# Performance work log

Measured on AMD Instinct MI355X. Metric: run time of the kernel, lower is better.

The kernel has to match this reference:

```python
import jax, jax.numpy as jnp
import numpy as np

D_MODEL, H, D_K, D_V = 512, 8, 64, 64
S_Q, S_KV = 2048, 2048


def setup_inputs() -> dict:
    key = jax.random.key(0)
    ks = jax.random.split(key, 11)
    sc = 0.02
    return {
        "embeddings": jax.random.normal(ks[0], (S_Q, D_MODEL), jnp.float32),
        "K": jax.random.normal(ks[1], (S_KV, D_MODEL), jnp.float32),
        "V": jax.random.normal(ks[2], (S_KV, D_MODEL), jnp.float32),
        # per-head projection weights (stacked over heads) + biases
        "Wq": jax.random.normal(ks[3], (H, D_MODEL, D_K), jnp.float32) * sc,
        "bq": jax.random.normal(ks[4], (H, D_K), jnp.float32) * sc,
        "Wk": jax.random.normal(ks[5], (H, D_MODEL, D_K), jnp.float32) * sc,
        "bk": jax.random.normal(ks[6], (H, D_K), jnp.float32) * sc,
        "Wv": jax.random.normal(ks[7], (H, D_MODEL, D_V), jnp.float32) * sc,
        "bv": jax.random.normal(ks[8], (H, D_V), jnp.float32) * sc,
        # final linear: [h*d_v -> d_model]
        "Wo": jax.random.normal(ks[9], (H * D_V, D_MODEL), jnp.float32) * sc,
        "bo": jax.random.normal(ks[10], (D_MODEL,), jnp.float32) * sc,
    }


def reference(embeddings, K, V, Wq, bq, Wk, bk, Wv, bv, Wo, bo):
    # Batched per-head projections (the original loops over h heads; math identical)
    q = jnp.einsum("sd,hdk->hsk", embeddings, Wq) + bq[:, None, :]  # [h, Sq, d_k]
    k = jnp.einsum("td,hdk->htk", K, Wk) + bk[:, None, :]           # [h, Skv, d_k]
    v = jnp.einsum("td,hdv->htv", V, Wv) + bv[:, None, :]           # [h, Skv, d_v]
    scores = jnp.einsum("hsk,htk->hst", q, k) / jnp.sqrt(jnp.asarray(D_K, q.dtype))
    attn = jax.nn.softmax(scores, axis=-1)                           # [h, Sq, Skv]
    out = jnp.einsum("hst,htv->hsv", attn, v)                        # [h, Sq, d_v]
    # torch.cat(results, dim=1): head 0's d_v columns first -> [Sq, h*d_v]
    concat = jnp.transpose(out, (1, 0, 2)).reshape(S_Q, H * D_V)
    return concat @ Wo + bo                                          # [Sq, d_model]
```

## Files before the change

### kernel.cpp

```cpp
#include <hip/hip_runtime.h>

#define SQ 2048
#define DM 512
#define NH 8
#define NSPLIT 4

typedef __bf16 bf16x8 __attribute__((ext_vector_type(8)));
typedef float f32x4 __attribute__((ext_vector_type(4)));
typedef unsigned short us8 __attribute__((ext_vector_type(8)));
typedef unsigned short us4 __attribute__((ext_vector_type(4)));

__device__ __forceinline__ unsigned short f2bf(float f) {
    unsigned u = __builtin_bit_cast(unsigned, f);
    u += 0x7fffu + ((u >> 16) & 1u);
    return (unsigned short)(u >> 16);
}
__device__ __forceinline__ float bf2f(unsigned short u) {
    return __builtin_bit_cast(float, (unsigned)u << 16);
}

__global__ __launch_bounds__(256) void convert_w(
    const float* __restrict__ Wq,  const float* __restrict__ Wk,  const float* __restrict__ Wv,
    const float* __restrict__ Wo,
    unsigned short* __restrict__ Wt,
    unsigned short* __restrict__ Woth, unsigned short* __restrict__ Wotl)
{
    const int b = blockIdx.x, tid = threadIdx.x;
    __shared__ float ld[64 * 68];
    float4* ld4 = reinterpret_cast<float4*>(ld);

    if (b < 192) {
        const int wi = b;
        const int idx = wi >> 3;
        const int kt = wi & 7;
        const int p = idx >> 3, h = idx & 7;
        const float* src = ((p == 0) ? Wq : (p == 1) ? Wk : Wv)
                         + (size_t)h * 512 * 64 + (size_t)kt * 64 * 64;
        unsigned short* dst = Wt + (size_t)idx * 64 * 512 + kt * 64;
        const int rr = tid >> 4, c4 = tid & 15;
        #pragma unroll
        for (int it = 0; it < 4; it++) {
            int r = rr + 16 * it;
            ld4[r * 17 + c4] = reinterpret_cast<const float4*>(src + (size_t)r * 64)[c4];
        }
        __syncthreads();
        #pragma unroll
        for (int it = 0; it < 2; it++) {
            int slot = tid + it * 256;
            int n = slot >> 3, g = slot & 7;
            us8 o;
            #pragma unroll
            for (int i = 0; i < 8; i++)
                o[i] = f2bf(ld[(g * 8 + i) * 68 + n]);
            *reinterpret_cast<us8*>(dst + (size_t)n * 512 + g * 8) = o;
        }
    } else {
        const int ti = b - 192;
        const int kt = ti >> 3, nt = ti & 7;
        const float* src = Wo + (size_t)kt * 64 * 512 + nt * 64;
        const int rr = tid >> 4, c4 = tid & 15;
        #pragma unroll
        for (int it = 0; it < 4; it++) {
            int r = rr + 16 * it;
            ld4[r * 17 + c4] = reinterpret_cast<const float4*>(src + (size_t)r * 512)[c4];
        }
        __syncthreads();
        #pragma unroll
        for (int it = 0; it < 2; it++) {
            int slot = tid + it * 256;
            int n = slot >> 3, g = slot & 7;
            us8 oh, ol;
            #pragma unroll
            for (int i = 0; i < 8; i++) {
                float v = ld[(g * 8 + i) * 68 + n];
                unsigned short hi = f2bf(v);
                oh[i] = hi;
                ol[i] = f2bf(v - bf2f(hi));
            }
            size_t doff = (size_t)(nt * 64 + n) * 512 + kt * 64 + g * 8;
            *reinterpret_cast<us8*>(Woth + doff) = oh;
            *reinterpret_cast<us8*>(Wotl + doff) = ol;
        }
    }
}

__global__ __launch_bounds__(256) void qkv_mfma(
    const float* __restrict__ emb, const float* __restrict__ Kin,
    const float* __restrict__ Vin, const unsigned short* __restrict__ Wt,
    const float* __restrict__ bq, const float* __restrict__ bk, const float* __restrict__ bv,
    unsigned short* __restrict__ qo, unsigned short* __restrict__ ko, unsigned short* __restrict__ vo)
{
    const int p = blockIdx.z, h = blockIdx.y, s0 = blockIdx.x * 64;
    const float* X = (p == 0) ? emb : (p == 1) ? Kin : Vin;
    const unsigned short* W = Wt + (size_t)(p * 8 + h) * 64 * 512;
    const float* B = ((p == 0) ? bq : (p == 1) ? bk : bv) + h * 64;

    const int tid = threadIdx.x;
    const int w = tid >> 6, lane = tid & 63, cl = lane & 15, q4 = lane >> 4;
    const int sr = tid >> 3, sg = tid & 7;

    __shared__ unsigned short As[2][64 * 72];
    __shared__ unsigned short Bs[2][64 * 72];

    #pragma unroll
    for (int it = 0; it < 2; it++) {
        int r = sr + 32 * it;
        const float4* xs = reinterpret_cast<const float4*>(&X[(size_t)(s0 + r) * 512 + sg * 8]);
        float4 f0 = xs[0], f1 = xs[1];
        us8 o;
        o[0] = f2bf(f0.x); o[1] = f2bf(f0.y); o[2] = f2bf(f0.z); o[3] = f2bf(f0.w);
        o[4] = f2bf(f1.x); o[5] = f2bf(f1.y); o[6] = f2bf(f1.z); o[7] = f2bf(f1.w);
        *reinterpret_cast<us8*>(&As[0][r * 72 + sg * 8]) = o;
        *reinterpret_cast<float4*>(&Bs[0][r * 72 + sg * 8]) =
            *reinterpret_cast<const float4*>(&W[(size_t)r * 512 + sg * 8]);
    }

    f32x4 acc[4] = {};

    for (int c = 0; c < 8; c++) {
        __syncthreads();
        const int buf = c & 1;
        const bool more = (c + 1 < 8);
        float4 ar[2][2], br[2];
        if (more) {
            #pragma unroll
            for (int it = 0; it < 2; it++) {
                int r = sr + 32 * it;
                const float4* xs = reinterpret_cast<const float4*>(
                    &X[(size_t)(s0 + r) * 512 + (c + 1) * 64 + sg * 8]);
                ar[it][0] = xs[0];
                ar[it][1] = xs[1];
                br[it] = *reinterpret_cast<const float4*>(
                    &W[(size_t)r * 512 + (c + 1) * 64 + sg * 8]);
            }
        }

        bf16x8 a0 = *reinterpret_cast<const bf16x8*>(&As[buf][(16 * w + cl) * 72 + q4 * 8]);
        bf16x8 a1 = *reinterpret_cast<const bf16x8*>(&As[buf][(16 * w + cl) * 72 + 32 + q4 * 8]);
        #pragma unroll
        for (int nn = 0; nn < 4; nn++) {
            bf16x8 b0 = *reinterpret_cast<const bf16x8*>(&Bs[buf][(16 * nn + cl) * 72 + q4 * 8]);
            bf16x8 b1 = *reinterpret_cast<const bf16x8*>(&Bs[buf][(16 * nn + cl) * 72 + 32 + q4 * 8]);
            acc[nn] = __builtin_amdgcn_mfma_f32_16x16x32_bf16(a0, b0, acc[nn], 0, 0, 0);
            acc[nn] = __builtin_amdgcn_mfma_f32_16x16x32_bf16(a1, b1, acc[nn], 0, 0, 0);
        }

        if (more) {
            const int nbuf = buf ^ 1;
            #pragma unroll
            for (int it = 0; it < 2; it++) {
                int r = sr + 32 * it;
                us8 o;
                o[0] = f2bf(ar[it][0].x); o[1] = f2bf(ar[it][0].y);
                o[2] = f2bf(ar[it][0].z); o[3] = f2bf(ar[it][0].w);
                o[4] = f2bf(ar[it][1].x); o[5] = f2bf(ar[it][1].y);
                o[6] = f2bf(ar[it][1].z); o[7] = f2bf(ar[it][1].w);
                *reinterpret_cast<us8*>(&As[nbuf][r * 72 + sg * 8]) = o;
                *reinterpret_cast<float4*>(&Bs[nbuf][r * 72 + sg * 8]) = br[it];
            }
        }
    }

    if (p == 0) {
        const float QSCALE = 0.125f * 1.4426950408889634f;
        #pragma unroll
        for (int nn = 0; nn < 4; nn++) {
            int col = 16 * nn + cl;
            float bb = B[col];
            #pragma unroll
            for (int r = 0; r < 4; r++)
                qo[((size_t)h * SQ + s0 + 16 * w + q4 * 4 + r) * 64 + col] =
                    f2bf((acc[nn][r] + bb) * QSCALE);
        }
    } else if (p == 1) {
        #pragma unroll
        for (int nn = 0; nn < 4; nn++) {
            int col = 16 * nn + cl;
            float bb = B[col];
            #pragma unroll
            for (int r = 0; r < 4; r++)
                ko[((size_t)h * SQ + s0 + 16 * w + q4 * 4 + r) * 64 + col] =
                    f2bf(acc[nn][r] + bb);
        }
    } else {
        #pragma unroll
        for (int nn = 0; nn < 4; nn++) {
            int col = 16 * nn + cl;
            float bb = B[col];
            ushort4 o;
            o.x = f2bf(acc[nn][0] + bb);
            o.y = f2bf(acc[nn][1] + bb);
            o.z = f2bf(acc[nn][2] + bb);
            o.w = f2bf(acc[nn][3] + bb);
            *reinterpret_cast<ushort4*>(
                vo + ((size_t)h * 64 + col) * SQ + s0 + 16 * w + q4 * 4) = o;
        }
    }
}

#define PW 72

__global__ __launch_bounds__(256, 4) void attn_fwd(
    const unsigned short* __restrict__ qbf,
    const unsigned short* __restrict__ kbf,
    const unsigned short* __restrict__ vbf,
    float* __restrict__ Opart,
    float* __restrict__ lpart)
{
    const int h = blockIdx.y, s0 = blockIdx.x * 64, z = blockIdx.z;
    const int tid = threadIdx.x;
    const int w = tid >> 6, lane = tid & 63, cl = lane & 15, q4 = lane >> 4;
    const int NT = SQ / 64 / NSPLIT;
    const int t0 = z * NT;

    __shared__ unsigned short Ks[2][64 * PW];
    __shared__ unsigned short Vs[2][64 * PW];

    bf16x8 aq0 = *reinterpret_cast<const bf16x8*>(
        &qbf[((size_t)h * SQ + s0 + 16 * w + cl) * 64 + q4 * 8]);
    bf16x8 aq1 = *reinterpret_cast<const bf16x8*>(
        &qbf[((size_t)h * SQ + s0 + 16 * w + cl) * 64 + 32 + q4 * 8]);

    const int sr = tid >> 3, sg = tid & 7;
    const int kapA = 32 * (sg >> 2) + 16 * (sg & 1) + 4 * ((sg >> 1) & 1);

    #pragma unroll
    for (int it = 0; it < 2; it++) {
        int r = sr + 32 * it;
        *reinterpret_cast<float4*>(&Ks[0][r * PW + sg * 8]) =
            *reinterpret_cast<const float4*>(&kbf[((size_t)h * SQ + t0 * 64 + r) * 64 + sg * 8]);
        us8 vv = *reinterpret_cast<const us8*>(&vbf[((size_t)h * 64 + r) * SQ + t0 * 64 + sg * 8]);
        *reinterpret_cast<us4*>(&Vs[0][r * PW + kapA]) =
            __builtin_shufflevector(vv, vv, 0, 1, 2, 3);
        *reinterpret_cast<us4*>(&Vs[0][r * PW + kapA + 8]) =
            __builtin_shufflevector(vv, vv, 4, 5, 6, 7);
    }

    f32x4 o_acc[4] = {};
    float lsum = 0.f;

    for (int tl = 0; tl < NT; tl++) {
        __syncthreads();
        const int buf = tl & 1;
        const bool more = (tl + 1 < NT);
        float4 kr[2];
        us8 vr[2];
        if (more) {
            #pragma unroll
            for (int it = 0; it < 2; it++) {
                int r = sr + 32 * it;
                kr[it] = *reinterpret_cast<const float4*>(
                    &kbf[((size_t)h * SQ + (t0 + tl + 1) * 64 + r) * 64 + sg * 8]);
                vr[it] = *reinterpret_cast<const us8*>(
                    &vbf[((size_t)h * 64 + r) * SQ + (t0 + tl + 1) * 64 + sg * 8]);
            }
        }

        f32x4 s_acc[4] = {};
        #pragma unroll
        for (int nn = 0; nn < 4; nn++) {
            bf16x8 k0 = *reinterpret_cast<const bf16x8*>(&Ks[buf][(16 * nn + cl) * PW + q4 * 8]);
            bf16x8 k1 = *reinterpret_cast<const bf16x8*>(&Ks[buf][(16 * nn + cl) * PW + 32 + q4 * 8]);
            s_acc[nn] = __builtin_amdgcn_mfma_f32_16x16x32_bf16(k0, aq0, s_acc[nn], 0, 0, 0);
            s_acc[nn] = __builtin_amdgcn_mfma_f32_16x16x32_bf16(k1, aq1, s_acc[nn], 0, 0, 0);
        }

        bf16x8 ap0, ap1;
        #pragma unroll
        for (int nn = 0; nn < 4; nn++) {
            #pragma unroll
            for (int r = 0; r < 4; r++) {
                float pv = __builtin_amdgcn_exp2f(s_acc[nn][r]);
                lsum += pv;
                if (nn < 2) ap0[nn * 4 + r] = (__bf16)pv;
                else        ap1[(nn - 2) * 4 + r] = (__bf16)pv;
            }
        }

        #pragma unroll
        for (int nn = 0; nn < 4; nn++) {
            bf16x8 b0 = *reinterpret_cast<const bf16x8*>(&Vs[buf][(16 * nn + cl) * PW + q4 * 8]);
            bf16x8 b1 = *reinterpret_cast<const bf16x8*>(&Vs[buf][(16 * nn + cl) * PW + 32 + q4 * 8]);
            o_acc[nn] = __builtin_amdgcn_mfma_f32_16x16x32_bf16(ap0, b0, o_acc[nn], 0, 0, 0);
            o_acc[nn] = __builtin_amdgcn_mfma_f32_16x16x32_bf16(ap1, b1, o_acc[nn], 0, 0, 0);
        }

        if (more) {
            const int nbuf = buf ^ 1;
            #pragma unroll
            for (int it = 0; it < 2; it++) {
                int r = sr + 32 * it;
                *reinterpret_cast<float4*>(&Ks[nbuf][r * PW + sg * 8]) = kr[it];
                *reinterpret_cast<us4*>(&Vs[nbuf][r * PW + kapA]) =
                    __builtin_shufflevector(vr[it], vr[it], 0, 1, 2, 3);
                *reinterpret_cast<us4*>(&Vs[nbuf][r * PW + kapA + 8]) =
                    __builtin_shufflevector(vr[it], vr[it], 4, 5, 6, 7);
            }
        }
    }

    lsum += __shfl_xor(lsum, 16);
    lsum += __shfl_xor(lsum, 32);

    const size_t zb = (size_t)(z * NH + h);
    if (q4 == 0)
        lpart[zb * SQ + s0 + 16 * w + cl] = lsum;

    #pragma unroll
    for (int nn = 0; nn < 4; nn++)
        #pragma unroll
        for (int r = 0; r < 4; r++)
            Opart[(zb * SQ + s0 + 16 * w + q4 * 4 + r) * 64 + 16 * nn + cl] = o_acc[nn][r];
}

__global__ __launch_bounds__(256) void attn_combine(
    const float* __restrict__ Opart, const float* __restrict__ lpart,
    unsigned short* __restrict__ athi, unsigned short* __restrict__ atlo)
{
    const int gid = blockIdx.x * 256 + threadIdx.x;
    const int s = gid >> 6, oct = gid & 63;
    const int col0 = oct * 8, h = col0 >> 6, dv0 = col0 & 63;

    float l = 0.f;
    #pragma unroll
    for (int z = 0; z < NSPLIT; z++)
        l += lpart[(size_t)(z * NH + h) * SQ + s];
    const float inv = 1.0f / l;

    float o[8] = {};
    #pragma unroll
    for (int z = 0; z < NSPLIT; z++) {
        const float4* base = reinterpret_cast<const float4*>(
            Opart + ((size_t)(z * NH + h) * SQ + s) * 64 + dv0);
        float4 a = base[0], bq = base[1];
        o[0] += a.x; o[1] += a.y; o[2] += a.z; o[3] += a.w;
        o[4] += bq.x; o[5] += bq.y; o[6] += bq.z; o[7] += bq.w;
    }
    us8 hi, lo;
    #pragma unroll
    for (int i = 0; i < 8; i++) {
        float v = o[i] * inv;
        unsigned short hb = f2bf(v);
        hi[i] = hb;
        lo[i] = f2bf(v - bf2f(hb));
    }
    *reinterpret_cast<us8*>(athi + (size_t)s * DM + col0) = hi;
    *reinterpret_cast<us8*>(atlo + (size_t)s * DM + col0) = lo;
}

__global__ __launch_bounds__(256) void out_proj(
    const unsigned short* __restrict__ ah, const unsigned short* __restrict__ al,
    const unsigned short* __restrict__ Wh, const unsigned short* __restrict__ Wl,
    const float* __restrict__ bo, float* __restrict__ out)
{
    const int s0 = blockIdx.x * 64, n0 = blockIdx.y * 64;
    const int tid = threadIdx.x;
    const int w = tid >> 6, lane = tid & 63, cl = lane & 15, q4 = lane >> 4;
    const int sr = tid >> 3, sg = tid & 7;

    __shared__ unsigned short Ah[2][64 * 72], Al[2][64 * 72];
    __shared__ unsigned short Bh[2][64 * 72], Bl[2][64 * 72];

    #pragma unroll
    for (int it = 0; it < 2; it++) {
        int r = sr + 32 * it;
        *reinterpret_cast<float4*>(&Ah[0][r * 72 + sg * 8]) =
            *reinterpret_cast<const float4*>(&ah[(size_t)(s0 + r) * 512 + sg * 8]);
        *reinterpret_cast<float4*>(&Al[0][r * 72 + sg * 8]) =
            *reinterpret_cast<const float4*>(&al[(size_t)(s0 + r) * 512 + sg * 8]);
        *reinterpret_cast<float4*>(&Bh[0][r * 72 + sg * 8]) =
            *reinterpret_cast<const float4*>(&Wh[(size_t)(n0 + r) * 512 + sg * 8]);
        *reinterpret_cast<float4*>(&Bl[0][r * 72 + sg * 8]) =
            *reinterpret_cast<const float4*>(&Wl[(size_t)(n0 + r) * 512 + sg * 8]);
    }

    f32x4 acc[4] = {};

    for (int c = 0; c < 8; c++) {
        __syncthreads();
        const int buf = c & 1;
        const bool more = (c + 1 < 8);
        float4 ahr[2], alr[2], bhr[2], blr[2];
        if (more) {
            #pragma unroll
            for (int it = 0; it < 2; it++) {
                int r = sr + 32 * it;
                int off = (c + 1) * 64 + sg * 8;
                ahr[it] = *reinterpret_cast<const float4*>(&ah[(size_t)(s0 + r) * 512 + off]);
                alr[it] = *reinterpret_cast<const float4*>(&al[(size_t)(s0 + r) * 512 + off]);
                bhr[it] = *reinterpret_cast<const float4*>(&Wh[(size_t)(n0 + r) * 512 + off]);
                blr[it] = *reinterpret_cast<const float4*>(&Wl[(size_t)(n0 + r) * 512 + off]);
            }
        }

        bf16x8 ah0 = *reinterpret_cast<const bf16x8*>(&Ah[buf][(16 * w + cl) * 72 + q4 * 8]);
        bf16x8 ah1 = *reinterpret_cast<const bf16x8*>(&Ah[buf][(16 * w + cl) * 72 + 32 + q4 * 8]);
        bf16x8 al0 = *reinterpret_cast<const bf16x8*>(&Al[buf][(16 * w + cl) * 72 + q4 * 8]);
        bf16x8 al1 = *reinterpret_cast<const bf16x8*>(&Al[buf][(16 * w + cl) * 72 + 32 + q4 * 8]);
        #pragma unroll
        for (int nn = 0; nn < 4; nn++) {
            bf16x8 bh0 = *reinterpret_cast<const bf16x8*>(&Bh[buf][(16 * nn + cl) * 72 + q4 * 8]);
            bf16x8 bh1 = *reinterpret_cast<const bf16x8*>(&Bh[buf][(16 * nn + cl) * 72 + 32 + q4 * 8]);
            bf16x8 bl0 = *reinterpret_cast<const bf16x8*>(&Bl[buf][(16 * nn + cl) * 72 + q4 * 8]);
            bf16x8 bl1 = *reinterpret_cast<const bf16x8*>(&Bl[buf][(16 * nn + cl) * 72 + 32 + q4 * 8]);
            acc[nn] = __builtin_amdgcn_mfma_f32_16x16x32_bf16(ah0, bh0, acc[nn], 0, 0, 0);
            acc[nn] = __builtin_amdgcn_mfma_f32_16x16x32_bf16(ah1, bh1, acc[nn], 0, 0, 0);
            acc[nn] = __builtin_amdgcn_mfma_f32_16x16x32_bf16(ah0, bl0, acc[nn], 0, 0, 0);
            acc[nn] = __builtin_amdgcn_mfma_f32_16x16x32_bf16(ah1, bl1, acc[nn], 0, 0, 0);
            acc[nn] = __builtin_amdgcn_mfma_f32_16x16x32_bf16(al0, bh0, acc[nn], 0, 0, 0);
            acc[nn] = __builtin_amdgcn_mfma_f32_16x16x32_bf16(al1, bh1, acc[nn], 0, 0, 0);
        }

        if (more) {
            const int nbuf = buf ^ 1;
            #pragma unroll
            for (int it = 0; it < 2; it++) {
                int r = sr + 32 * it;
                *reinterpret_cast<float4*>(&Ah[nbuf][r * 72 + sg * 8]) = ahr[it];
                *reinterpret_cast<float4*>(&Al[nbuf][r * 72 + sg * 8]) = alr[it];
                *reinterpret_cast<float4*>(&Bh[nbuf][r * 72 + sg * 8]) = bhr[it];
                *reinterpret_cast<float4*>(&Bl[nbuf][r * 72 + sg * 8]) = blr[it];
            }
        }
    }

    #pragma unroll
    for (int nn = 0; nn < 4; nn++) {
        int col = n0 + 16 * nn + cl;
        float bb = bo[col];
        #pragma unroll
        for (int r = 0; r < 4; r++)
            out[(size_t)(s0 + 16 * w + q4 * 4 + r) * DM + col] = acc[nn][r] + bb;
    }
}

extern "C" void kernel_launch(void* const* d_in, const int* in_sizes, int n_in,
                              void* d_out, int out_size, void* d_ws, size_t ws_size,
                              hipStream_t stream) {
    const float* emb = (const float*)d_in[0];
    const float* Kin = (const float*)d_in[1];
    const float* Vin = (const float*)d_in[2];
    const float* Wq  = (const float*)d_in[3];
    const float* bq  = (const float*)d_in[4];
    const float* Wk  = (const float*)d_in[5];
    const float* bk  = (const float*)d_in[6];
    const float* Wv  = (const float*)d_in[7];
    const float* bv  = (const float*)d_in[8];
    const float* Wo  = (const float*)d_in[9];
    const float* bo  = (const float*)d_in[10];
    float* out = (float*)d_out;

    unsigned short* p = (unsigned short*)d_ws;
    unsigned short* Wt   = p; p += (size_t)24 * 64 * 512;
    unsigned short* Woth = p; p += (size_t)512 * 512;
    unsigned short* Wotl = p; p += (size_t)512 * 512;
    unsigned short* qbf  = p; p += (size_t)NH * SQ * 64;
    unsigned short* kbf  = p; p += (size_t)NH * SQ * 64;
    unsigned short* vbf  = p; p += (size_t)NH * SQ * 64;
    unsigned short* athi = p; p += (size_t)SQ * DM;
    unsigned short* atlo = p; p += (size_t)SQ * DM;
    float* Opart = (float*)p;
    float* lpart = Opart + (size_t)NSPLIT * NH * SQ * 64;

    convert_w<<<256, 256, 0, stream>>>(Wq, Wk, Wv, Wo, Wt, Woth, Wotl);
    qkv_mfma<<<dim3(32, 8, 3), 256, 0, stream>>>(emb, Kin, Vin, Wt, bq, bk, bv,
                                                 qbf, kbf, vbf);
    attn_fwd<<<dim3(32, 8, NSPLIT), 256, 0, stream>>>(qbf, kbf, vbf, Opart, lpart);
    attn_combine<<<512, 256, 0, stream>>>(Opart, lpart, athi, atlo);
    out_proj<<<dim3(32, 8), 256, 0, stream>>>(athi, atlo, Woth, Wotl, bo, out);
}
```

Baseline: 120.5 us.

## Split attention KV tiles across wave pairs with two query subtiles per wave

Each wave now processes 32 query rows (two 16-row subtiles) against one of two KV tiles staged together, so each K/V fragment read from LDS feeds two MFMAs instead of one. The two wave pairs reduce their partial O and row sums through shared memory at the end. The register-prefetch double buffer is dropped in favour of synchronous staging of two tiles per iteration, which exposes global load latency and doubles accumulator register use.

```diff
diff --git a/kernel.cpp b/kernel.cpp
--- a/kernel.cpp
+++ b/kernel.cpp
@@ -210,107 +210,128 @@
     const int h = blockIdx.y, s0 = blockIdx.x * 64, z = blockIdx.z;
     const int tid = threadIdx.x;
     const int w = tid >> 6, lane = tid & 63, cl = lane & 15, q4 = lane >> 4;
+    const int qh = w >> 1, tp = w & 1;
     const int NT = SQ / 64 / NSPLIT;
     const int t0 = z * NT;
 
-    __shared__ unsigned short Ks[2][64 * PW];
-    __shared__ unsigned short Vs[2][64 * PW];
-
-    bf16x8 aq0 = *reinterpret_cast<const bf16x8*>(
-        &qbf[((size_t)h * SQ + s0 + 16 * w + cl) * 64 + q4 * 8]);
-    bf16x8 aq1 = *reinterpret_cast<const bf16x8*>(
-        &qbf[((size_t)h * SQ + s0 + 16 * w + cl) * 64 + 32 + q4 * 8]);
+    __shared__ unsigned short SH[4 * 64 * PW];
+
+    bf16x8 aq[2][2];
+    #pragma unroll
+    for (int qs = 0; qs < 2; qs++) {
+        const unsigned short* qb =
+            &qbf[((size_t)h * SQ + s0 + 32 * qh + 16 * qs + cl) * 64 + q4 * 8];
+        aq[qs][0] = *reinterpret_cast<const bf16x8*>(qb);
+        aq[qs][1] = *reinterpret_cast<const bf16x8*>(qb + 32);
+    }
 
     const int sr = tid >> 3, sg = tid & 7;
     const int kapA = 32 * (sg >> 2) + 16 * (sg & 1) + 4 * ((sg >> 1) & 1);
 
-    #pragma unroll
-    for (int it = 0; it < 2; it++) {
-        int r = sr + 32 * it;
-        *reinterpret_cast<float4*>(&Ks[0][r * PW + sg * 8]) =
-            *reinterpret_cast<const float4*>(&kbf[((size_t)h * SQ + t0 * 64 + r) * 64 + sg * 8]);
-        us8 vv = *reinterpret_cast<const us8*>(&vbf[((size_t)h * 64 + r) * SQ + t0 * 64 + sg * 8]);
-        *reinterpret_cast<us4*>(&Vs[0][r * PW + kapA]) =
-            __builtin_shufflevector(vv, vv, 0, 1, 2, 3);
-        *reinterpret_cast<us4*>(&Vs[0][r * PW + kapA + 8]) =
-            __builtin_shufflevector(vv, vv, 4, 5, 6, 7);
-    }
-
-    f32x4 o_acc[4] = {};
-    float lsum = 0.f;
-
-    for (int tl = 0; tl < NT; tl++) {
+    auto stage = [&](int par, int t) {
+        unsigned short* Kd = &SH[par * 64 * PW];
+        unsigned short* Vd = &SH[(2 + par) * 64 * PW];
+        #pragma unroll
+        for (int it = 0; it < 2; it++) {
+            int r = sr + 32 * it;
+            *reinterpret_cast<float4*>(&Kd[r * PW + sg * 8]) =
+                *reinterpret_cast<const float4*>(&kbf[((size_t)h * SQ + t * 64 + r) * 64 + sg * 8]);
+            us8 vv = *reinterpret_cast<const us8*>(&vbf[((size_t)h * 64 + r) * SQ + t * 64 + sg * 8]);
+            *reinterpret_cast<us4*>(&Vd[r * PW + kapA]) =
+                __builtin_shufflevector(vv, vv, 0, 1, 2, 3);
+            *reinterpret_cast<us4*>(&Vd[r * PW + kapA + 8]) =
+                __builtin_shufflevector(vv, vv, 4, 5, 6, 7);
+        }
+    };
+
+    stage(0, t0);
+    stage(1, t0 + 1);
+    __syncthreads();
+
+    f32x4 o_acc[2][4] = {};
+    float lsum[2] = {};
+    const unsigned short* Kb = &SH[tp * 64 * PW];
+    const unsigned short* Vb = &SH[(2 + tp) * 64 * PW];
+
+    for (int pr = 0; pr < NT / 2; pr++) {
+        f32x4 s_acc[2][4] = {};
+        #pragma unroll
+        for (int nn = 0; nn < 4; nn++) {
+            bf16x8 k0 = *reinterpret_cast<const bf16x8*>(&Kb[(16 * nn + cl) * PW + q4 * 8]);
+            bf16x8 k1 = *reinterpret_cast<const bf16x8*>(&Kb[(16 * nn + cl) * PW + 32 + q4 * 8]);
+            #pragma unroll
+            for (int qs = 0; qs < 2; qs++) {
+                s_acc[qs][nn] = __builtin_amdgcn_mfma_f32_16x16x32_bf16(k0, aq[qs][0], s_acc[qs][nn], 0, 0, 0);
+                s_acc[qs][nn] = __builtin_amdgcn_mfma_f32_16x16x32_bf16(k1, aq[qs][1], s_acc[qs][nn], 0, 0, 0);
+            }
+        }
+
+        bf16x8 ap[2][2];
+        #pragma unroll
+        for (int qs = 0; qs < 2; qs++)
+            #pragma unroll
+            for (int nn = 0; nn < 4; nn++)
+                #pragma unroll
+                for (int r = 0; r < 4; r++) {
+                    float pv = __builtin_amdgcn_exp2f(s_acc[qs][nn][r]);
+                    lsum[qs] += pv;
+                    ap[qs][nn >> 1][(nn & 1) * 4 + r] = (__bf16)pv;
+                }
+
+        #pragma unroll
+        for (int nn = 0; nn < 4; nn++) {
+            bf16x8 b0 = *reinterpret_cast<const bf16x8*>(&Vb[(16 * nn + cl) * PW + q4 * 8]);
+            bf16x8 b1 = *reinterpret_cast<const bf16x8*>(&Vb[(16 * nn + cl) * PW + 32 + q4 * 8]);
+            #pragma unroll
+            for (int qs = 0; qs < 2; qs++) {
+                o_acc[qs][nn] = __builtin_amdgcn_mfma_f32_16x16x32_bf16(ap[qs][0], b0, o_acc[qs][nn], 0, 0, 0);
+                o_acc[qs][nn] = __builtin_amdgcn_mfma_f32_16x16x32_bf16(ap[qs][1], b1, o_acc[qs][nn], 0, 0, 0);
+            }
+        }
+
         __syncthreads();
-        const int buf = tl & 1;
-        const bool more = (tl + 1 < NT);
-        float4 kr[2];
-        us8 vr[2];
-        if (more) {
-            #pragma unroll
-            for (int it = 0; it < 2; it++) {
-                int r = sr + 32 * it;
-                kr[it] = *reinterpret_cast<const float4*>(
-                    &kbf[((size_t)h * SQ + (t0 + tl + 1) * 64 + r) * 64 + sg * 8]);
-                vr[it] = *reinterpret_cast<const us8*>(
-                    &vbf[((size_t)h * 64 + r) * SQ + (t0 + tl + 1) * 64 + sg * 8]);
-            }
-        }
-
-        f32x4 s_acc[4] = {};
-        #pragma unroll
-        for (int nn = 0; nn < 4; nn++) {
-            bf16x8 k0 = *reinterpret_cast<const bf16x8*>(&Ks[buf][(16 * nn + cl) * PW + q4 * 8]);
-            bf16x8 k1 = *reinterpret_cast<const bf16x8*>(&Ks[buf][(16 * nn + cl) * PW + 32 + q4 * 8]);
-            s_acc[nn] = __builtin_amdgcn_mfma_f32_16x16x32_bf16(k0, aq0, s_acc[nn], 0, 0, 0);
-            s_acc[nn] = __builtin_amdgcn_mfma_f32_16x16x32_bf16(k1, aq1, s_acc[nn], 0, 0, 0);
-        }
-
-        bf16x8 ap0, ap1;
-        #pragma unroll
-        for (int nn = 0; nn < 4; nn++) {
-            #pragma unroll
-            for (int r = 0; r < 4; r++) {
-                float pv = __builtin_amdgcn_exp2f(s_acc[nn][r]);
-                lsum += pv;
-                if (nn < 2) ap0[nn * 4 + r] = (__bf16)pv;
-                else        ap1[(nn - 2) * 4 + r] = (__bf16)pv;
-            }
-        }
-
-        #pragma unroll
-        for (int nn = 0; nn < 4; nn++) {
-            bf16x8 b0 = *reinterpret_cast<const bf16x8*>(&Vs[buf][(16 * nn + cl) * PW + q4 * 8]);
-            bf16x8 b1 = *reinterpret_cast<const bf16x8*>(&Vs[buf][(16 * nn + cl) * PW + 32 + q4 * 8]);
-            o_acc[nn] = __builtin_amdgcn_mfma_f32_16x16x32_bf16(ap0, b0, o_acc[nn], 0, 0, 0);
-            o_acc[nn] = __builtin_amdgcn_mfma_f32_16x16x32_bf16(ap1, b1, o_acc[nn], 0, 0, 0);
-        }
-
-        if (more) {
-            const int nbuf = buf ^ 1;
-            #pragma unroll
-            for (int it = 0; it < 2; it++) {
-                int r = sr + 32 * it;
-                *reinterpret_cast<float4*>(&Ks[nbuf][r * PW + sg * 8]) = kr[it];
-                *reinterpret_cast<us4*>(&Vs[nbuf][r * PW + kapA]) =
-                    __builtin_shufflevector(vr[it], vr[it], 0, 1, 2, 3);
-                *reinterpret_cast<us4*>(&Vs[nbuf][r * PW + kapA + 8]) =
-                    __builtin_shufflevector(vr[it], vr[it], 4, 5, 6, 7);
-            }
-        }
-    }
-
-    lsum += __shfl_xor(lsum, 16);
-    lsum += __shfl_xor(lsum, 32);
-
-    const size_t zb = (size_t)(z * NH + h);
-    if (q4 == 0)
-        lpart[zb * SQ + s0 + 16 * w + cl] = lsum;
-
-    #pragma unroll
-    for (int nn = 0; nn < 4; nn++)
-        #pragma unroll
-        for (int r = 0; r < 4; r++)
-            Opart[(zb * SQ + s0 + 16 * w + q4 * 4 + r) * 64 + 16 * nn + cl] = o_acc[nn][r];
+        if (pr + 1 < NT / 2) {
+            stage(0, t0 + 2 * pr + 2);
+            stage(1, t0 + 2 * pr + 3);
+            __syncthreads();
+        }
+    }
+
+    __syncthreads();
+    float* Ox = reinterpret_cast<float*>(SH);
+    float* Lx = Ox + 4096;
+    if (tp == 1) {
+        #pragma unroll
+        for (int qs = 0; qs < 2; qs++) {
+            #pragma unroll
+            for (int nn = 0; nn < 4; nn++)
+                *reinterpret_cast<f32x4*>(&Ox[(((qh * 2 + qs) * 4 + nn) * 256) + lane * 4]) =
+                    o_acc[qs][nn];
+            Lx[(qh * 2 + qs) * 64 + lane] = lsum[qs];
+        }
+    }
+    __syncthreads();
+    if (tp == 0) {
+        const size_t zb = (size_t)(z * NH + h);
+        #pragma unroll
+        for (int qs = 0; qs < 2; qs++) {
+            #pragma unroll
+            for (int nn = 0; nn < 4; nn++)
+                o_acc[qs][nn] += *reinterpret_cast<const f32x4*>(
+                    &Ox[(((qh * 2 + qs) * 4 + nn) * 256) + lane * 4]);
+            float v = lsum[qs] + Lx[(qh * 2 + qs) * 64 + lane];
+            v += __shfl_xor(v, 16);
+            v += __shfl_xor(v, 32);
+            if (q4 == 0)
+                lpart[zb * SQ + s0 + 32 * qh + 16 * qs + cl] = v;
+            #pragma unroll
+            for (int nn = 0; nn < 4; nn++)
+                #pragma unroll
+                for (int r = 0; r < 4; r++)
+                    Opart[(zb * SQ + s0 + 32 * qh + 16 * qs + 4 * q4 + r) * 64 + 16 * nn + cl] =
+                        o_acc[qs][nn][r];
+        }
+    }
 }
 
 __global__ __launch_bounds__(256) void attn_combine(
```

New measurement: 126.4 us. 4.8% more time.
